# Kernel optimization log

Measured on AMD Instinct MI355X. Metric: run time of the kernel, lower is better.

## Reference

```python
import jax, jax.numpy as jnp
import numpy as np

N, D, N_SIGMAS = 4096, 128, 75

def _pairwise_sq_dist(x):
    # squared euclidean distances, [N, N]
    sq = jnp.sum(x * x, axis=1)
    d2 = sq[:, None] + sq[None, :] - 2.0 * (x @ x.T)
    return jnp.maximum(d2, 0.0)

def setup_inputs() -> dict:
    key = jax.random.key(0)
    kx, ky = jax.random.split(key)
    x = jax.random.normal(kx, (N, D), dtype=jnp.float32)
    # realistic label kernel: RBF over random 10-dim label embeddings
    y = jax.random.normal(ky, (N, 10), dtype=jnp.float32)
    label_kernel = jnp.exp(-_pairwise_sq_dist(y))
    return {"x": x, "label_kernel": label_kernel}

def reference(x, label_kernel):
    n = x.shape[0]
    d2 = _pairwise_sq_dist(x)              # [N, N] squared distances
    nz = d2 > 0
    # safe sqrt (avoid nan grads on diagonal zeros)
    dist = jnp.where(nz, jnp.sqrt(jnp.where(nz, d2, 1.0)), 0.0)
    # mean of nonzero distances (distance[distance != 0].mean())
    mean_distance = jnp.sum(dist) / jnp.sum(nz).astype(x.dtype)
    lo = 0.1 * mean_distance
    hi = 10.0 * mean_distance
    step = (hi - lo) / N_SIGMAS
    sigmas = lo + step * jnp.arange(N_SIGMAS, dtype=x.dtype)  # np.arange equivalent

    label_norm = jnp.linalg.norm(label_kernel)

    def alignment_loss(sigma):
        K = jnp.exp(-d2 / (sigma * sigma))
        return jnp.sum(K * label_kernel) / (jnp.linalg.norm(K) * label_norm)

    losses = jax.lax.map(alignment_loss, sigmas)   # sequential sigma sweep
    sigma_opt = sigmas[jnp.argmax(losses)]         # first max, like np.argwhere(...).item()

    A = jnp.exp(-d2 / (sigma_opt * sigma_opt)) / n
    return A
```

## Files before the change

kernel.cpp:

```cpp
#include <hip/hip_runtime.h>
#include <hip/hip_bf16.h>

#define NN 4096
#define DD 128
#define NS 75
#define TOT (NN * NN)

#define BT 128
#define NBD2 (NN / BT)
#define GRID_D2 (NBD2 * (NBD2 + 1) / 2)

#define SB 64
#define NBSW (NN / SB)
#define NTILES (NBSW * (NBSW + 1) / 2)
#define GRID_SW (NTILES / 2)

typedef float v2f __attribute__((ext_vector_type(2)));
typedef float f32x4 __attribute__((ext_vector_type(4)));
typedef short bf16x8 __attribute__((ext_vector_type(8)));

__device__ __forceinline__ float fexp2(float v) { return __builtin_amdgcn_exp2f(v); }

__device__ __forceinline__ void gload_lds16(const void* g, void* l) {
    __builtin_amdgcn_global_load_lds(
        (const __attribute__((address_space(1))) unsigned int*)g,
        (__attribute__((address_space(3))) unsigned int*)l,
        16, 0, 0);
}

template <int CTRL>
__device__ __forceinline__ float dpp_add(float x) {
    int y = __builtin_amdgcn_update_dpp(0, __float_as_int(x), CTRL, 0xf, 0xf, true);
    return x + __int_as_float(y);
}
__device__ __forceinline__ float wave_sum(float x) {
    x = dpp_add<0x111>(x);
    x = dpp_add<0x112>(x);
    x = dpp_add<0x114>(x);
    x = dpp_add<0x118>(x);
    x = dpp_add<0x142>(x);
    x = dpp_add<0x143>(x);
    return x;
}

__device__ __forceinline__ void tri_decode(int t, int nb, int& bi, int& bj) {
    int b = 0, rem = t;
    while (rem >= nb - b) { rem -= nb - b; ++b; }
    bi = b; bj = b + rem;
}

__device__ __forceinline__ void cvt_split(const float4& v0, const float4& v1,
                                          bf16x8& hi, bf16x8& lo) {
    float f[8] = {v0.x, v0.y, v0.z, v0.w, v1.x, v1.y, v1.z, v1.w};
#pragma unroll
    for (int j = 0; j < 8; ++j) {
        unsigned b = __float_as_uint(f[j]);
        hi[j] = (short)(b >> 16);
        float l = f[j] - __uint_as_float(b & 0xFFFF0000u);
        lo[j] = (short)(__float_as_uint(l) >> 16);
    }
}

__device__ __forceinline__ const unsigned short* xrow_st(const float* d2, int i, int lo) {
    return (const unsigned short*)(d2 + (size_t)(2048 + lo * 128 + (i >> 5)) * NN + (i & 31) * 64);
}
__device__ __forceinline__ unsigned short* xrow_st_w(float* d2, int i, int lo) {
    return (unsigned short*)(d2 + (size_t)(2048 + lo * 128 + (i >> 5)) * NN + (i & 31) * 64);
}

__device__ __forceinline__ int coarse_window(const double* KL, const double* KK) {
    double best = -1.0;
    int bk = 0;
    for (int k = 0; k < 25; ++k) {
        double loss = KL[k] / sqrt(KK[k]);
        if (loss > best) { best = loss; bk = k; }
    }
    int wv = 3 * bk - 2;
    if (wv < 0) wv = 0;
    if (wv > NS - 5) wv = NS - 5;
    return wv;
}

#define WS_DSUM 0
#define WS_NZC  8
#define WS_KL   16
#define WS_KK   (16 + 256)
#define WS_SQ   (16 + 512)
#define WS_CSIG (WS_SQ + 4 * NN)

__global__ void k_rowsq(const float* __restrict__ x, float* __restrict__ sq,
                        double* __restrict__ dsum, unsigned long long* __restrict__ nzc) {
    int tid = blockIdx.x * blockDim.x + threadIdx.x;
    if (tid == 0) { *dsum = 0.0; *nzc = 0ull; }
    if (tid < NN) {
        const float4* row = (const float4*)(x + (size_t)tid * DD);
        float s = 0.f;
#pragma unroll
        for (int i = 0; i < DD / 4; ++i) {
            float4 v = row[i];
            s += v.x * v.x + v.y * v.y + v.z * v.z + v.w * v.w;
        }
        sq[tid] = s;
    }
}

__global__ void k_cvt(const float* __restrict__ x, float* __restrict__ d2) {
    int t = blockIdx.x * blockDim.x + threadIdx.x;
    int i  = t >> 4;
    int k8 = (t & 15) * 8;
    const float* p = x + (size_t)i * DD + k8;
    float4 v0 = *(const float4*)p;
    float4 v1 = *(const float4*)(p + 4);
    bf16x8 hi, lo;
    cvt_split(v0, v1, hi, lo);
    *(bf16x8*)(xrow_st_w(d2, i, 0) + k8) = hi;
    *(bf16x8*)(xrow_st_w(d2, i, 1) + k8) = lo;
}

__launch_bounds__(512, 2)
__global__ void k_d2(const float* __restrict__ x, const float* __restrict__ sq,
                     float* __restrict__ d2, double* __restrict__ dsum,
                     unsigned long long* __restrict__ nzc) {
    __shared__ float st[64][132];
    __shared__ double red_d[8];
    __shared__ int red_n[8];

    int bi, bj;
    tri_decode(blockIdx.x, NBD2, bi, bj);
    const int r0 = bi * BT, c0 = bj * BT;
    const int tid = threadIdx.x;
    const int l = tid & 63, wid = tid >> 6;
    const int wr = wid >> 1, wc = wid & 1;
    const int lr = l & 15;
    const int lk = (l >> 4) * 8;
    const int l4 = (l >> 4) * 4;

    const int arow = r0 + wr * 32 + lr;
    const int brow = c0 + wc * 64 + lr;

    f32x4 acc[2][4];
#pragma unroll
    for (int a = 0; a < 2; ++a)
#pragma unroll
        for (int b = 0; b < 4; ++b) acc[a][b] = (f32x4){0.f, 0.f, 0.f, 0.f};

#pragma unroll
    for (int kc = 0; kc < 4; ++kc) {
        const int k0 = kc * 32 + lk;
        bf16x8 ah[2], al[2], bh[4], bl[4];
#pragma unroll
        for (int a = 0; a < 2; ++a) {
            ah[a] = *(const bf16x8*)(xrow_st(d2, arow + a * 16, 0) + k0);
            al[a] = *(const bf16x8*)(xrow_st(d2, arow + a * 16, 1) + k0);
        }
#pragma unroll
        for (int b = 0; b < 4; ++b) {
            bh[b] = *(const bf16x8*)(xrow_st(d2, brow + b * 16, 0) + k0);
            bl[b] = *(const bf16x8*)(xrow_st(d2, brow + b * 16, 1) + k0);
        }
#pragma unroll
        for (int a = 0; a < 2; ++a)
#pragma unroll
            for (int b = 0; b < 4; ++b) {
                acc[a][b] = __builtin_amdgcn_mfma_f32_16x16x32_bf16(ah[a], bh[b], acc[a][b], 0, 0, 0);
                acc[a][b] = __builtin_amdgcn_mfma_f32_16x16x32_bf16(ah[a], bl[b], acc[a][b], 0, 0, 0);
                acc[a][b] = __builtin_amdgcn_mfma_f32_16x16x32_bf16(al[a], bh[b], acc[a][b], 0, 0, 0);
            }
    }

    float myd = 0.f;
    int myn = 0;
#pragma unroll
    for (int a = 0; a < 2; ++a) {
        const int grb = r0 + wr * 32 + a * 16 + l4;
        float4 sqr = *(const float4*)(sq + grb);
        float sr[4] = {sqr.x, sqr.y, sqr.z, sqr.w};
#pragma unroll
        for (int b = 0; b < 4; ++b) {
            const float sc = sq[c0 + wc * 64 + b * 16 + lr];
#pragma unroll
            for (int v = 0; v < 4; ++v) {
                float d = fmaxf(sr[v] + sc - 2.f * acc[a][b][v], 0.f);
                acc[a][b][v] = d;
                if (d > 0.f) { myd += sqrtf(d); ++myn; }
            }
        }
    }
    const int w = (bi == bj) ? 1 : 2;
    float sd = wave_sum(myd);
    float sn = wave_sum((float)myn);
    if (l == 63) { red_d[wid] = (double)sd; red_n[wid] = (int)sn; }

#pragma unroll
    for (int p = 0; p < 2; ++p) {
        __syncthreads();
        if ((wr >> 1) == p) {
            const int lrow = (wr & 1) * 32 + l4;
#pragma unroll
            for (int a = 0; a < 2; ++a)
#pragma unroll
                for (int b = 0; b < 4; ++b)
#pragma unroll
                    for (int v = 0; v < 4; ++v)
                        st[lrow + (a == 1 ? 16 : 0) + v][wc * 64 + b * 16 + lr] = acc[a][b][v];
        }
        __syncthreads();
#pragma unroll
        for (int q = 0; q < 4; ++q) {
            const int rr = q * 16 + (tid >> 5);
            const int cc = (tid & 31) * 4;
            *(f32x4*)(d2 + (size_t)(r0 + p * 64 + rr) * NN + c0 + cc) =
                *(const f32x4*)&st[rr][cc];
        }
    }

    if (tid == 0) {
        double td = 0.0;
        int tn = 0;
#pragma unroll
        for (int q = 0; q < 8; ++q) { td += red_d[q]; tn += red_n[q]; }
        atomicAdd(dsum, td * (double)w);
        atomicAdd(nzc, (unsigned long long)(tn * w));
    }
}

__global__ void k_sigmas(const double* __restrict__ dsum, const unsigned long long* __restrict__ nzc,
                         float* __restrict__ csig, double* __restrict__ KL, double* __restrict__ KK) {
    int t = threadIdx.x;
    float mean = (float)(*dsum / (double)(*nzc));
    float lo = 0.1f * mean;
    float hi = 10.0f * mean;
    float step = (hi - lo) / (float)NS;
    if (t < NS) {
        float s = lo + step * (float)t;
        csig[t] = (float)(1.4426950408889634 / ((double)s * (double)s));
    }
    if (t < 32) { KL[t] = 0.0; KK[t] = 0.0; }
}

template <bool ADD, int CH, int S0, int STRIDE, int NSLOT>
__device__ __forceinline__ void sweep_phase(const v2f* nd, const v2f* ll,
                                            const float* __restrict__ csig, int off,
                                            double part[4][2 * NSLOT],
                                            int wave, int lane, float w) {
    float c[CH];
#pragma unroll
    for (int s = 0; s < CH; ++s)
        c[s] = __int_as_float(__builtin_amdgcn_readfirstlane(
                   __float_as_int(csig[off + STRIDE * (S0 + s)])));
    v2f akl[CH], akk[CH];
#pragma unroll
    for (int s = 0; s < CH; ++s) { akl[s] = (v2f){0.f, 0.f}; akk[s] = (v2f){0.f, 0.f}; }

#pragma unroll
    for (int e = 0; e < 8; ++e) {
        v2f ndv = nd[e], L = ll[e];
#pragma unroll
        for (int s = 0; s < CH; ++s) {
            v2f arg = ndv * c[s];
            v2f K = {fexp2(arg.x), fexp2(arg.y)};
            akl[s] = __builtin_elementwise_fma(K, L, akl[s]);
            akk[s] = __builtin_elementwise_fma(K, K, akk[s]);
        }
    }

#pragma unroll
    for (int s = 0; s < CH; ++s) {
        float v1 = wave_sum(akl[s].x + akl[s].y);
        float v2 = wave_sum(akk[s].x + akk[s].y);
        if (lane == 63) {
            if (ADD) {
                part[wave][S0 + s]         += (double)(v1 * w);
                part[wave][NSLOT + S0 + s] += (double)(v2 * w);
            } else {
                part[wave][S0 + s]         = (double)(v1 * w);
                part[wave][NSLOT + S0 + s] = (double)(v2 * w);
            }
        }
    }
}

__device__ __forceinline__ void sweep_load_direct(const float* __restrict__ d2,
                                                  const float* __restrict__ lk,
                                                  int r0, int c0, v2f* nd, v2f* ll) {
    const int rr = threadIdx.x >> 4;
    const int c4 = (threadIdx.x & 15) * 4;
#pragma unroll
    for (int it = 0; it < 4; ++it) {
        size_t off = (size_t)(r0 + rr + 16 * it) * NN + c0 + c4;
        float4 dv = *(const float4*)(d2 + off);
        float4 lv = *(const float4*)(lk + off);
        nd[it * 2 + 0] = (v2f){-dv.x, -dv.y};
        nd[it * 2 + 1] = (v2f){-dv.z, -dv.w};
        ll[it * 2 + 0] = (v2f){lv.x, lv.y};
        ll[it * 2 + 1] = (v2f){lv.z, lv.w};
    }
}

__device__ __forceinline__ void sweep_prefetch(const float* __restrict__ d2,
                                               const float* __restrict__ lk,
                                               int r0, int c0, char* wbuf) {
    const int l = threadIdx.x & 63;
    const int wave4 = (threadIdx.x >> 6) * 4;
    const int rr = wave4 + (l >> 4);
    const int c4 = (l & 15) * 4;
#pragma unroll
    for (int q = 0; q < 4; ++q) {
        size_t off = (size_t)(r0 + rr + 16 * q) * NN + c0 + c4;
        gload_lds16(d2 + off, wbuf + q * 1024);
        gload_lds16(lk + off, wbuf + (4 + q) * 1024);
    }
}

__device__ __forceinline__ void sweep_unpack(const char* wbuf, v2f* nd, v2f* ll) {
    const int l = threadIdx.x & 63;
#pragma unroll
    for (int q = 0; q < 4; ++q) {
        f32x4 dv = *(const f32x4*)(wbuf + q * 1024 + l * 16);
        f32x4 lv = *(const f32x4*)(wbuf + (4 + q) * 1024 + l * 16);
        nd[q * 2 + 0] = (v2f){-dv[0], -dv[1]};
        nd[q * 2 + 1] = (v2f){-dv[2], -dv[3]};
        ll[q * 2 + 0] = (v2f){lv[0], lv[1]};
        ll[q * 2 + 1] = (v2f){lv[2], lv[3]};
    }
}

__launch_bounds__(256, 3)
__global__ void k_sweep_coarse(const float* __restrict__ d2, const float* __restrict__ lk,
                               const float* __restrict__ csig, double* __restrict__ KL,
                               double* __restrict__ KK) {
    __shared__ char pbuf[4][8192];
    __shared__ double part[4][50];
    const int lane = threadIdx.x & 63, wave = threadIdx.x >> 6;

    int t0 = blockIdx.x * 2, t1 = t0 + 1;
    int bi0, bj0, bi1, bj1;
    tri_decode(t0, NBSW, bi0, bj0);
    tri_decode(t1, NBSW, bi1, bj1);
    const float w0 = (bi0 == bj0) ? 1.f : 2.f;
    const float w1 = (bi1 == bj1) ? 1.f : 2.f;

    sweep_prefetch(d2, lk, bi1 * SB, bj1 * SB, &pbuf[wave][0]);
    v2f nd[8], ll[8];
    sweep_load_direct(d2, lk, bi0 * SB, bj0 * SB, nd, ll);

    sweep_phase<false, 13, 0, 3, 25>(nd, ll, csig, 0, part, wave, lane, w0);
    sweep_phase<false, 12, 13, 3, 25>(nd, ll, csig, 0, part, wave, lane, w0);

    asm volatile("s_waitcnt vmcnt(0)" ::: "memory");
    sweep_unpack(&pbuf[wave][0], nd, ll);

    sweep_phase<true, 13, 0, 3, 25>(nd, ll, csig, 0, part, wave, lane, w1);
    sweep_phase<true, 12, 13, 3, 25>(nd, ll, csig, 0, part, wave, lane, w1);

    __syncthreads();
    const int t = threadIdx.x;
    if (t < 50) {
        double v = part[0][t] + part[1][t] + part[2][t] + part[3][t];
        if (t < 25) atomicAdd(&KL[t], v);
        else        atomicAdd(&KK[t - 25], v);
    }
}

__launch_bounds__(256, 3)
__global__ void k_sweep_refine(const float* __restrict__ d2, const float* __restrict__ lk,
                               const float* __restrict__ csig, double* __restrict__ KL,
                               double* __restrict__ KK) {
    __shared__ char pbuf[4][8192];
    __shared__ double part[4][10];
    __shared__ int w0_sh;
    if (threadIdx.x == 0) w0_sh = coarse_window(KL, KK);
    const int lane = threadIdx.x & 63, wave = threadIdx.x >> 6;

    int t0 = blockIdx.x * 2, t1 = t0 + 1;
    int bi0, bj0, bi1, bj1;
    tri_decode(t0, NBSW, bi0, bj0);
    tri_decode(t1, NBSW, bi1, bj1);
    const float wt0 = (bi0 == bj0) ? 1.f : 2.f;
    const float wt1 = (bi1 == bj1) ? 1.f : 2.f;

    sweep_prefetch(d2, lk, bi1 * SB, bj1 * SB, &pbuf[wave][0]);
    v2f nd[8], ll[8];
    sweep_load_direct(d2, lk, bi0 * SB, bj0 * SB, nd, ll);
    __syncthreads();
    const int s0 = w0_sh;

    sweep_phase<false, 5, 0, 1, 5>(nd, ll, csig, s0, part, wave, lane, wt0);

    asm volatile("s_waitcnt vmcnt(0)" ::: "memory");
    sweep_unpack(&pbuf[wave][0], nd, ll);

    sweep_phase<true, 5, 0, 1, 5>(nd, ll, csig, s0, part, wave, lane, wt1);

    __syncthreads();
    const int t = threadIdx.x;
    if (t < 10) {
        double v = part[0][t] + part[1][t] + part[2][t] + part[3][t];
        if (t < 5) atomicAdd(&KL[25 + t], v);
        else       atomicAdd(&KK[25 + t - 5], v);
    }
}

__global__ void k_final(float* __restrict__ d2, const double* __restrict__ KL,
                        const double* __restrict__ KK, const float* __restrict__ csig) {
    __shared__ float st[64][68];
    __shared__ float cc_sh;
    if (threadIdx.x == 0) {
        int wv = coarse_window(KL, KK);
        double best = -1.0;
        int bk = 0;
        for (int k = 0; k < 5; ++k) {
            double loss = KL[25 + k] / sqrt(KK[25 + k]);
            if (loss > best) { best = loss; bk = k; }
        }
        cc_sh = csig[wv + bk];
    }
    __syncthreads();
    const float cc = cc_sh;
    const float inv_n = 1.0f / (float)NN;

    int ti, tj;
    tri_decode(blockIdx.x, NBSW, ti, tj);
    const int r0 = ti * SB, c0 = tj * SB;
    const int tid = threadIdx.x;

#pragma unroll
    for (int q = 0; q < 4; ++q) {
        const int rr = q * 16 + (tid >> 4);
        const int cc4 = (tid & 15) * 4;
        float* p = d2 + (size_t)(r0 + rr) * NN + c0 + cc4;
        f32x4 v = *(const f32x4*)p;
        v[0] = fexp2(-v[0] * cc) * inv_n;
        v[1] = fexp2(-v[1] * cc) * inv_n;
        v[2] = fexp2(-v[2] * cc) * inv_n;
        v[3] = fexp2(-v[3] * cc) * inv_n;
        *(f32x4*)p = v;
        *(f32x4*)&st[rr][cc4] = v;
    }

    if (ti != tj) {
        __syncthreads();
#pragma unroll
        for (int q = 0; q < 4; ++q) {
            const int tc = q * 16 + (tid >> 4);
            const int rb = (tid & 15) * 4;
            f32x4 vv = {st[rb + 0][tc], st[rb + 1][tc], st[rb + 2][tc], st[rb + 3][tc]};
            *(f32x4*)(d2 + (size_t)(c0 + tc) * NN + r0 + rb) = vv;
        }
    }
}

extern "C" void kernel_launch(void* const* d_in, const int* in_sizes, int n_in,
                              void* d_out, int out_size, void* d_ws, size_t ws_size,
                              hipStream_t stream) {
    const float* x  = (const float*)d_in[0];
    const float* lk = (const float*)d_in[1];
    float* out = (float*)d_out;
    char* ws = (char*)d_ws;

    double* dsum = (double*)(ws + WS_DSUM);
    unsigned long long* nzc = (unsigned long long*)(ws + WS_NZC);
    double* KL = (double*)(ws + WS_KL);
    double* KK = (double*)(ws + WS_KK);
    float* sqv  = (float*)(ws + WS_SQ);
    float* csig = (float*)(ws + WS_CSIG);

    hipLaunchKernelGGL(k_rowsq, dim3(NN / 256), dim3(256), 0, stream, x, sqv, dsum, nzc);
    hipLaunchKernelGGL(k_cvt, dim3(256), dim3(256), 0, stream, x, out);
    hipLaunchKernelGGL(k_d2, dim3(GRID_D2), dim3(512), 0, stream, x, sqv, out, dsum, nzc);
    hipLaunchKernelGGL(k_sigmas, dim3(1), dim3(128), 0, stream, dsum, nzc, csig, KL, KK);
    hipLaunchKernelGGL(k_sweep_coarse, dim3(GRID_SW), dim3(256), 0, stream, out, lk, csig, KL, KK);
    hipLaunchKernelGGL(k_sweep_refine, dim3(GRID_SW), dim3(256), 0, stream, out, lk, csig, KL, KK);
    hipLaunchKernelGGL(k_final, dim3(NTILES), dim3(256), 0, stream, out, KL, KK, csig);
}
```

Baseline: 141.4 us.

## Shrink d2 tiles to 64x128 with per-wave weights; sweep four tiles per block

The distance kernel now uses 64x128 tiles with 256 threads instead of 128x128 tiles with 512 threads. It covers the upper triangle at a finer granularity, applying a per-wave weight of 0, 1 or 2 and skipping the lower-half store where needed. This is meant to cut work wasted on the diagonal and to raise occupancy. The coarse sweep now processes four tiles per block with a rolling LDS prefetch, which amortises block setup and overlaps loads with compute, but gives fewer blocks to spread across the CUs.

```diff
diff --git a/kernel.cpp b/kernel.cpp
--- a/kernel.cpp
+++ b/kernel.cpp
@@ -6,14 +6,15 @@
 #define NS 75
 #define TOT (NN * NN)
 
-#define BT 128
-#define NBD2 (NN / BT)
-#define GRID_D2 (NBD2 * (NBD2 + 1) / 2)
+#define NRT 64
+#define NCT2 32
+#define GRID_D2 1056
 
 #define SB 64
 #define NBSW (NN / SB)
 #define NTILES (NBSW * (NBSW + 1) / 2)
-#define GRID_SW (NTILES / 2)
+#define GRID_SWC (NTILES / 4)
+#define GRID_SWR (NTILES / 2)
 
 typedef float v2f __attribute__((ext_vector_type(2)));
 typedef float f32x4 __attribute__((ext_vector_type(4)));
@@ -47,6 +48,12 @@
     int b = 0, rem = t;
     while (rem >= nb - b) { rem -= nb - b; ++b; }
     bi = b; bj = b + rem;
+}
+
+__device__ __forceinline__ void d2_decode(int t, int& ti, int& tj2) {
+    int g = 0, rem = t;
+    while (rem >= NCT2 - (g >> 1)) { rem -= NCT2 - (g >> 1); ++g; }
+    ti = g; tj2 = (g >> 1) + rem;
 }
 
 __device__ __forceinline__ void cvt_split(const float4& v0, const float4& v1,
@@ -117,17 +124,17 @@
     *(bf16x8*)(xrow_st_w(d2, i, 1) + k8) = lo;
 }
 
-__launch_bounds__(512, 2)
+__launch_bounds__(256, 4)
 __global__ void k_d2(const float* __restrict__ x, const float* __restrict__ sq,
                      float* __restrict__ d2, double* __restrict__ dsum,
                      unsigned long long* __restrict__ nzc) {
     __shared__ float st[64][132];
-    __shared__ double red_d[8];
-    __shared__ int red_n[8];
-
-    int bi, bj;
-    tri_decode(blockIdx.x, NBD2, bi, bj);
-    const int r0 = bi * BT, c0 = bj * BT;
+    __shared__ double red_d[4];
+    __shared__ int red_n[4];
+
+    int ti, tj2;
+    d2_decode(blockIdx.x, ti, tj2);
+    const int r0 = ti * 64, c0 = tj2 * 128;
     const int tid = threadIdx.x;
     const int l = tid & 63, wid = tid >> 6;
     const int wr = wid >> 1, wc = wid & 1;
@@ -137,6 +144,8 @@
 
     const int arow = r0 + wr * 32 + lr;
     const int brow = c0 + wc * 64 + lr;
+    const int tc_tile = 2 * tj2 + wc;
+    const int w_w = (tc_tile == ti) ? 1 : (tc_tile > ti ? 2 : 0);
 
     f32x4 acc[2][4];
 #pragma unroll
@@ -186,41 +195,42 @@
             }
         }
     }
-    const int w = (bi == bj) ? 1 : 2;
     float sd = wave_sum(myd);
     float sn = wave_sum((float)myn);
-    if (l == 63) { red_d[wid] = (double)sd; red_n[wid] = (int)sn; }
-
-#pragma unroll
-    for (int p = 0; p < 2; ++p) {
-        __syncthreads();
-        if ((wr >> 1) == p) {
-            const int lrow = (wr & 1) * 32 + l4;
-#pragma unroll
-            for (int a = 0; a < 2; ++a)
-#pragma unroll
-                for (int b = 0; b < 4; ++b)
-#pragma unroll
-                    for (int v = 0; v < 4; ++v)
-                        st[lrow + (a == 1 ? 16 : 0) + v][wc * 64 + b * 16 + lr] = acc[a][b][v];
-        }
-        __syncthreads();
+    if (l == 63) { red_d[wid] = (double)sd * w_w; red_n[wid] = (int)sn * w_w; }
+
+    const int srow = wr * 32 + l4;
+#pragma unroll
+    for (int a = 0; a < 2; ++a)
+#pragma unroll
+        for (int b = 0; b < 4; ++b)
+#pragma unroll
+            for (int v = 0; v < 4; ++v)
+                st[srow + a * 16 + v][wc * 64 + b * 16 + lr] = acc[a][b][v];
+    __syncthreads();
+
+    const bool lhalf = (2 * tj2 >= ti);
+    if (lhalf) {
+#pragma unroll
+        for (int q = 0; q < 8; ++q) {
+            const int rr = q * 8 + (tid >> 5);
+            const int cc = (tid & 31) * 4;
+            *(f32x4*)(d2 + (size_t)(r0 + rr) * NN + c0 + cc) = *(const f32x4*)&st[rr][cc];
+        }
+    } else {
 #pragma unroll
         for (int q = 0; q < 4; ++q) {
-            const int rr = q * 16 + (tid >> 5);
-            const int cc = (tid & 31) * 4;
-            *(f32x4*)(d2 + (size_t)(r0 + p * 64 + rr) * NN + c0 + cc) =
-                *(const f32x4*)&st[rr][cc];
+            const int rr = q * 16 + (tid >> 4);
+            const int cc = 64 + (tid & 15) * 4;
+            *(f32x4*)(d2 + (size_t)(r0 + rr) * NN + c0 + cc) = *(const f32x4*)&st[rr][cc];
         }
     }
 
     if (tid == 0) {
-        double td = 0.0;
-        int tn = 0;
-#pragma unroll
-        for (int q = 0; q < 8; ++q) { td += red_d[q]; tn += red_n[q]; }
-        atomicAdd(dsum, td * (double)w);
-        atomicAdd(nzc, (unsigned long long)(tn * w));
+        double td = red_d[0] + red_d[1] + red_d[2] + red_d[3];
+        int tn = red_n[0] + red_n[1] + red_n[2] + red_n[3];
+        atomicAdd(dsum, td);
+        atomicAdd(nzc, (unsigned long long)tn);
     }
 }
 
@@ -333,25 +343,41 @@
     __shared__ double part[4][50];
     const int lane = threadIdx.x & 63, wave = threadIdx.x >> 6;
 
-    int t0 = blockIdx.x * 2, t1 = t0 + 1;
-    int bi0, bj0, bi1, bj1;
-    tri_decode(t0, NBSW, bi0, bj0);
-    tri_decode(t1, NBSW, bi1, bj1);
-    const float w0 = (bi0 == bj0) ? 1.f : 2.f;
-    const float w1 = (bi1 == bj1) ? 1.f : 2.f;
-
-    sweep_prefetch(d2, lk, bi1 * SB, bj1 * SB, &pbuf[wave][0]);
+    int bi[4], bj[4];
+    float w[4];
+#pragma unroll
+    for (int i = 0; i < 4; ++i) {
+        tri_decode(blockIdx.x * 4 + i, NBSW, bi[i], bj[i]);
+        w[i] = (bi[i] == bj[i]) ? 1.f : 2.f;
+    }
+
+    sweep_prefetch(d2, lk, bi[1] * SB, bj[1] * SB, &pbuf[wave][0]);
     v2f nd[8], ll[8];
-    sweep_load_direct(d2, lk, bi0 * SB, bj0 * SB, nd, ll);
-
-    sweep_phase<false, 13, 0, 3, 25>(nd, ll, csig, 0, part, wave, lane, w0);
-    sweep_phase<false, 12, 13, 3, 25>(nd, ll, csig, 0, part, wave, lane, w0);
+    sweep_load_direct(d2, lk, bi[0] * SB, bj[0] * SB, nd, ll);
+
+    sweep_phase<false, 13, 0, 3, 25>(nd, ll, csig, 0, part, wave, lane, w[0]);
+    sweep_phase<false, 12, 13, 3, 25>(nd, ll, csig, 0, part, wave, lane, w[0]);
 
     asm volatile("s_waitcnt vmcnt(0)" ::: "memory");
     sweep_unpack(&pbuf[wave][0], nd, ll);
-
-    sweep_phase<true, 13, 0, 3, 25>(nd, ll, csig, 0, part, wave, lane, w1);
-    sweep_phase<true, 12, 13, 3, 25>(nd, ll, csig, 0, part, wave, lane, w1);
+    asm volatile("s_waitcnt lgkmcnt(0)" ::: "memory");
+    __builtin_amdgcn_sched_barrier(0);
+    sweep_prefetch(d2, lk, bi[2] * SB, bj[2] * SB, &pbuf[wave][0]);
+    sweep_phase<true, 13, 0, 3, 25>(nd, ll, csig, 0, part, wave, lane, w[1]);
+    sweep_phase<true, 12, 13, 3, 25>(nd, ll, csig, 0, part, wave, lane, w[1]);
+
+    asm volatile("s_waitcnt vmcnt(0)" ::: "memory");
+    sweep_unpack(&pbuf[wave][0], nd, ll);
+    asm volatile("s_waitcnt lgkmcnt(0)" ::: "memory");
+    __builtin_amdgcn_sched_barrier(0);
+    sweep_prefetch(d2, lk, bi[3] * SB, bj[3] * SB, &pbuf[wave][0]);
+    sweep_phase<true, 13, 0, 3, 25>(nd, ll, csig, 0, part, wave, lane, w[2]);
+    sweep_phase<true, 12, 13, 3, 25>(nd, ll, csig, 0, part, wave, lane, w[2]);
+
+    asm volatile("s_waitcnt vmcnt(0)" ::: "memory");
+    sweep_unpack(&pbuf[wave][0], nd, ll);
+    sweep_phase<true, 13, 0, 3, 25>(nd, ll, csig, 0, part, wave, lane, w[3]);
+    sweep_phase<true, 12, 13, 3, 25>(nd, ll, csig, 0, part, wave, lane, w[3]);
 
     __syncthreads();
     const int t = threadIdx.x;
@@ -467,9 +493,9 @@
 
     hipLaunchKernelGGL(k_rowsq, dim3(NN / 256), dim3(256), 0, stream, x, sqv, dsum, nzc);
     hipLaunchKernelGGL(k_cvt, dim3(256), dim3(256), 0, stream, x, out);
-    hipLaunchKernelGGL(k_d2, dim3(GRID_D2), dim3(512), 0, stream, x, sqv, out, dsum, nzc);
+    hipLaunchKernelGGL(k_d2, dim3(GRID_D2), dim3(256), 0, stream, x, sqv, out, dsum, nzc);
     hipLaunchKernelGGL(k_sigmas, dim3(1), dim3(128), 0, stream, dsum, nzc, csig, KL, KK);
-    hipLaunchKernelGGL(k_sweep_coarse, dim3(GRID_SW), dim3(256), 0, stream, out, lk, csig, KL, KK);
-    hipLaunchKernelGGL(k_sweep_refine, dim3(GRID_SW), dim3(256), 0, stream, out, lk, csig, KL, KK);
+    hipLaunchKernelGGL(k_sweep_coarse, dim3(GRID_SWC), dim3(256), 0, stream, out, lk, csig, KL, KK);
+    hipLaunchKernelGGL(k_sweep_refine, dim3(GRID_SWR), dim3(256), 0, stream, out, lk, csig, KL, KK);
     hipLaunchKernelGGL(k_final, dim3(NTILES), dim3(256), 0, stream, out, KL, KK, csig);
 }
```

New measurement: 154.9 us. 9.6% more time.
